# Optimization experiments

Hardware: AMD Instinct MI355X
Metric: run time of the kernel (lower is better)

Reference implementation:

```python
import jax, jax.numpy as jnp
import numpy as np

EMB_DIM = 2048
N_HEADS = 16
HEAD_DIM = EMB_DIM // N_HEADS
B, S = 4, 2048


def setup_inputs() -> dict:
    key = jax.random.key(0)
    kx, kq, kk, kv, ko = jax.random.split(key, 5)
    scale = 0.02
    return {
        "x": jax.random.normal(kx, (B, S, EMB_DIM), dtype=jnp.float32),
        "Wq": jax.random.normal(kq, (EMB_DIM, EMB_DIM), dtype=jnp.float32) * scale,
        "Wk": jax.random.normal(kk, (EMB_DIM, EMB_DIM), dtype=jnp.float32) * scale,
        "Wv": jax.random.normal(kv, (EMB_DIM, EMB_DIM), dtype=jnp.float32) * scale,
        "Wo": jax.random.normal(ko, (EMB_DIM, EMB_DIM), dtype=jnp.float32) * scale,
        "bo": jnp.zeros((EMB_DIM,), dtype=jnp.float32),
    }


def _split_heads(t):
    # [B, S, E] -> [B, H, S, Dh]
    b, s, _ = t.shape
    return t.reshape(b, s, N_HEADS, HEAD_DIM).transpose(0, 2, 1, 3)


def reference(x, Wq, Wk, Wv, Wo, bo):
    # torch nn.Linear: y = x @ W.T (no bias for qkv, bias for out_proj)
    q = _split_heads(x @ Wq.T)  # [B, H, S, Dh]
    k = _split_heads(x @ Wk.T)
    v = _split_heads(x @ Wv.T)

    scores = jnp.einsum("bhqd,bhkd->bhqk", q, k)  # [B, H, S, S]
    q_pos = jnp.arange(S)
    k_pos = jnp.arange(S)
    causal_mask = q_pos[:, None] < k_pos[None, :]  # True => future token, masked
    scores = jnp.where(causal_mask, -jnp.inf, scores)
    attn = jax.nn.softmax(scores / np.sqrt(HEAD_DIM).astype(np.float32), axis=-1)
    # dropout rate 0 (eval) -> identity
    ctx = jnp.einsum("bhqk,bhkd->bhqd", attn, v)  # [B, H, S, Dh]
    ctx = ctx.transpose(0, 2, 1, 3).reshape(B, S, EMB_DIM)
    return ctx @ Wo.T + bo
```

## Files before the change

### kernel.cpp

```cpp
#include <hip/hip_runtime.h>
#include <math.h>

#define EMB 2048
#define HD 128
#define SEQ 2048
#define MTOT 8192

typedef __bf16 bf16x8 __attribute__((ext_vector_type(8)));
typedef float floatx4 __attribute__((ext_vector_type(4)));

__device__ __forceinline__ unsigned short f2bf(float f) {
    unsigned u = __float_as_uint(f);
    return (unsigned short)((u + 0x7FFFu + ((u >> 16) & 1u)) >> 16);
}

__device__ __forceinline__ void gl_lds16(const void* g, void* lds) {
    __builtin_amdgcn_global_load_lds(
        (const __attribute__((address_space(1))) unsigned int*)g,
        (__attribute__((address_space(3))) unsigned int*)lds,
        16, 0, 0);
}

__global__ void cast_all_kernel(const float* __restrict__ x,
                                const float* __restrict__ w0,
                                const float* __restrict__ w1,
                                const float* __restrict__ w2,
                                const float* __restrict__ w3,
                                unsigned short* __restrict__ xb,
                                unsigned short* __restrict__ wb0,
                                unsigned short* __restrict__ wb1,
                                unsigned short* __restrict__ wb2,
                                unsigned short* __restrict__ wb3)
{
    const int XN4 = MTOT * EMB / 4;
    const int WN4 = EMB * EMB / 4;
    int i = blockIdx.x * blockDim.x + threadIdx.x;
    const float* src; unsigned short* dst; int off;
    if (i < XN4) { src = x; dst = xb; off = i; }
    else {
        int j = i - XN4;
        int wsel = j >> 20;
        off = j & (WN4 - 1);
        switch (wsel) {
            case 0: src = w0; dst = wb0; break;
            case 1: src = w1; dst = wb1; break;
            case 2: src = w2; dst = wb2; break;
            default: src = w3; dst = wb3; break;
        }
    }
    float4 v = reinterpret_cast<const float4*>(src)[off];
    ushort4 o;
    o.x = f2bf(v.x); o.y = f2bf(v.y); o.z = f2bf(v.z); o.w = f2bf(v.w);
    reinterpret_cast<ushort4*>(dst)[off] = o;
}

template<bool OUT_F32>
__global__ __launch_bounds__(256, 2)
void gemm_bt(const unsigned short* __restrict__ A,
             const unsigned short* __restrict__ Bw0,
             const unsigned short* __restrict__ Bw1,
             const unsigned short* __restrict__ Bw2,
             void* __restrict__ Cout0,
             void* __restrict__ Cout1,
             void* __restrict__ Cout2,
             const float* __restrict__ bias,
             int M, int N, int K, float scale0)
{
    __shared__ __align__(16) unsigned short sA[128][32];
    __shared__ __align__(16) unsigned short sB[128][32];

    const unsigned short* Bw = (blockIdx.z == 0) ? Bw0 : (blockIdx.z == 1) ? Bw1 : Bw2;
    void* Cout = (blockIdx.z == 0) ? Cout0 : (blockIdx.z == 1) ? Cout1 : Cout2;
    const float osc = (blockIdx.z == 0) ? scale0 : 1.0f;

    const int tid  = threadIdx.x;
    const int lane = tid & 63;
    const int wave = tid >> 6;
    const int wm = wave >> 1, wn = wave & 1;
    const int col  = lane & 15;
    const int quad = lane >> 4;

    const int m0 = blockIdx.y * 128;
    const int n0 = blockIdx.x * 128;

    floatx4 acc[4][4];
    #pragma unroll
    for (int i = 0; i < 4; i++)
        #pragma unroll
        for (int j = 0; j < 4; j++)
            #pragma unroll
            for (int r = 0; r < 4; r++) acc[i][j][r] = 0.0f;

    for (int k0 = 0; k0 < K; k0 += 32) {
        #pragma unroll
        for (int i = 0; i < 2; i++) {
            int c = tid + i * 256;
            int row = c >> 2, cc = (c & 3) * 8;
            char* ldsA = (char*)sA + (size_t)(i * 256 + wave * 64) * 16;
            char* ldsB = (char*)sB + (size_t)(i * 256 + wave * 64) * 16;
            gl_lds16(A  + (size_t)(m0 + row) * K + k0 + cc, ldsA);
            gl_lds16(Bw + (size_t)(n0 + row) * K + k0 + cc, ldsB);
        }
        __syncthreads();

        bf16x8 af[4], bfr[4];
        #pragma unroll
        for (int mi = 0; mi < 4; mi++)
            af[mi] = *reinterpret_cast<const bf16x8*>(&sA[wm*64 + mi*16 + col][quad*8]);
        #pragma unroll
        for (int ni = 0; ni < 4; ni++)
            bfr[ni] = *reinterpret_cast<const bf16x8*>(&sB[wn*64 + ni*16 + col][quad*8]);

        #pragma unroll
        for (int mi = 0; mi < 4; mi++)
            #pragma unroll
            for (int ni = 0; ni < 4; ni++)
                acc[mi][ni] = __builtin_amdgcn_mfma_f32_16x16x32_bf16(
                                  af[mi], bfr[ni], acc[mi][ni], 0, 0, 0);
        __syncthreads();
    }

    #pragma unroll
    for (int mi = 0; mi < 4; mi++) {
        #pragma unroll
        for (int ni = 0; ni < 4; ni++) {
            #pragma unroll
            for (int r = 0; r < 4; r++) {
                int row = m0 + wm*64 + mi*16 + quad*4 + r;
                int cg  = n0 + wn*64 + ni*16 + col;
                float v = acc[mi][ni][r];
                if (OUT_F32) {
                    float bb = bias ? bias[cg] : 0.0f;
                    reinterpret_cast<float*>(Cout)[(size_t)row * N + cg] = v + bb;
                } else {
                    reinterpret_cast<unsigned short*>(Cout)[(size_t)row * N + cg] = f2bf(v * osc);
                }
            }
        }
    }
}

__global__ __launch_bounds__(256, 2)
void flash_attn(const unsigned short* __restrict__ Q,
                const unsigned short* __restrict__ Kg,
                const unsigned short* __restrict__ Vg,
                unsigned short* __restrict__ O)
{
    __shared__ __align__(16) unsigned short sK[64 * 128];
    __shared__ __align__(16) unsigned short sVt[128][72];
    __shared__ __align__(16) unsigned short sP[4][16 * 72];

    const int tid  = threadIdx.x;
    const int lane = tid & 63;
    const int w    = tid >> 6;
    const int col  = lane & 15;
    const int quad = lane >> 4;

    const int h = blockIdx.y;
    const int b = blockIdx.z;
    const size_t rowbase = (size_t)b * SEQ;
    const int hoff = h * HD;

    unsigned short* sPw = sP[w];

    const int vk4 = (tid & 15) * 4;
    const int vd0 = (tid >> 4) * 8;

    #pragma unroll
    for (int phase = 0; phase < 2; phase++) {
        const int qsb = phase ? (int)blockIdx.x : (SEQ/128 - 1) - (int)blockIdx.x;
        const int qbase = qsb * 128;
        const int qg0 = qbase + w*32 + col;
        const int qg1 = qg0 + 16;

        bf16x8 qf[2][4];
        {
            const unsigned short* qr0 = Q + (rowbase + qg0) * EMB + hoff;
            const unsigned short* qr1 = Q + (rowbase + qg1) * EMB + hoff;
            #pragma unroll
            for (int ks = 0; ks < 4; ks++) {
                qf[0][ks] = *reinterpret_cast<const bf16x8*>(qr0 + ks*32 + quad*8);
                qf[1][ks] = *reinterpret_cast<const bf16x8*>(qr1 + ks*32 + quad*8);
            }
        }

        floatx4 oacc[2][8];
        #pragma unroll
        for (int g = 0; g < 2; g++)
            #pragma unroll
            for (int ni = 0; ni < 8; ni++)
                #pragma unroll
                for (int r = 0; r < 4; r++) oacc[g][ni][r] = 0.0f;
        float l_i[2] = {0.0f, 0.0f};

        const int ktmax = qbase / 64 + 1;
        for (int kt = 0; kt <= ktmax; kt++) {
            const int k0 = kt * 64;
            #pragma unroll
            for (int i = 0; i < 4; i++) {
                int c = tid + i * 256;
                int key = c >> 4;
                int dblk = (c & 15) ^ (key & 7);
                char* ldsK = (char*)sK + (size_t)(i * 256 + w * 64) * 16;
                gl_lds16(Kg + (rowbase + k0 + key) * EMB + hoff + dblk * 8, ldsK);
            }
            {
                unsigned short va[4][8];
                #pragma unroll
                for (int kk = 0; kk < 4; kk++)
                    *reinterpret_cast<int4*>(va[kk]) =
                        *reinterpret_cast<const int4*>(Vg + (rowbase + k0 + vk4 + kk) * EMB + hoff + vd0);
                #pragma unroll
                for (int j = 0; j < 8; j++) {
                    ushort4 o;
                    o.x = va[0][j]; o.y = va[1][j]; o.z = va[2][j]; o.w = va[3][j];
                    *reinterpret_cast<ushort4*>(&sVt[vd0 + j][vk4]) = o;
                }
            }
            __syncthreads();

            if (k0 <= qbase + w*32 + 31) {
                floatx4 sc[2][4];
                #pragma unroll
                for (int g = 0; g < 2; g++)
                    #pragma unroll
                    for (int ni = 0; ni < 4; ni++)
                        #pragma unroll
                        for (int r = 0; r < 4; r++) sc[g][ni][r] = 0.0f;
                #pragma unroll
                for (int ni = 0; ni < 4; ni++) {
                    #pragma unroll
                    for (int ks = 0; ks < 4; ks++) {
                        int u = (ni*16 + col) * 16 + ((ks*4 + quad) ^ (col & 7));
                        bf16x8 kf = *reinterpret_cast<const bf16x8*>(&sK[u * 8]);
                        sc[0][ni] = __builtin_amdgcn_mfma_f32_16x16x32_bf16(kf, qf[0][ks], sc[0][ni], 0, 0, 0);
                        sc[1][ni] = __builtin_amdgcn_mfma_f32_16x16x32_bf16(kf, qf[1][ks], sc[1][ni], 0, 0, 0);
                    }
                }

                const bool need_mask = (k0 + 63 > qbase + w*32);
                bf16x8 pf[2][2];

                #pragma unroll
                for (int g = 0; g < 2; g++) {
                    const int qg = (g == 0) ? qg0 : qg1;
                    if (need_mask) {
                        #pragma unroll
                        for (int ni = 0; ni < 4; ni++)
                            #pragma unroll
                            for (int r = 0; r < 4; r++) {
                                int key = k0 + ni*16 + quad*4 + r;
                                if (key > qg) sc[g][ni][r] = -1e30f;
                            }
                    }
                    float rsum = 0.0f;
                    #pragma unroll
                    for (int ni = 0; ni < 4; ni++) {
                        float p0 = __expf(sc[g][ni][0]);
                        float p1 = __expf(sc[g][ni][1]);
                        float p2 = __expf(sc[g][ni][2]);
                        float p3 = __expf(sc[g][ni][3]);
                        rsum += (p0 + p1) + (p2 + p3);
                        ushort4 pk;
                        pk.x = f2bf(p0); pk.y = f2bf(p1); pk.z = f2bf(p2); pk.w = f2bf(p3);
                        *reinterpret_cast<ushort4*>(&sPw[col*72 + ni*16 + quad*4]) = pk;
                    }
                    l_i[g] += rsum;
                    #pragma unroll
                    for (int ks = 0; ks < 2; ks++)
                        pf[g][ks] = *reinterpret_cast<const bf16x8*>(&sPw[col*72 + ks*32 + quad*8]);
                }

                #pragma unroll
                for (int ni = 0; ni < 8; ni++) {
                    #pragma unroll
                    for (int ks = 0; ks < 2; ks++) {
                        bf16x8 vf = *reinterpret_cast<const bf16x8*>(&sVt[ni*16 + col][ks*32 + quad*8]);
                        oacc[0][ni] = __builtin_amdgcn_mfma_f32_16x16x32_bf16(vf, pf[0][ks], oacc[0][ni], 0, 0, 0);
                        oacc[1][ni] = __builtin_amdgcn_mfma_f32_16x16x32_bf16(vf, pf[1][ks], oacc[1][ni], 0, 0, 0);
                    }
                }
            }
            __syncthreads();
        }

        #pragma unroll
        for (int g = 0; g < 2; g++) {
            const int qg = (g == 0) ? qg0 : qg1;
            float l = l_i[g];
            l += __shfl_xor(l, 16);
            l += __shfl_xor(l, 32);
            float inv = 1.0f / l;
            #pragma unroll
            for (int ni = 0; ni < 8; ni++) {
                ushort4 o4;
                o4.x = f2bf(oacc[g][ni][0] * inv);
                o4.y = f2bf(oacc[g][ni][1] * inv);
                o4.z = f2bf(oacc[g][ni][2] * inv);
                o4.w = f2bf(oacc[g][ni][3] * inv);
                *reinterpret_cast<ushort4*>(O + (rowbase + qg) * EMB + hoff + ni*16 + quad*4) = o4;
            }
        }
    }
}

extern "C" void kernel_launch(void* const* d_in, const int* in_sizes, int n_in,
                              void* d_out, int out_size, void* d_ws, size_t ws_size,
                              hipStream_t stream)
{
    const float* x  = (const float*)d_in[0];
    const float* Wq = (const float*)d_in[1];
    const float* Wk = (const float*)d_in[2];
    const float* Wv = (const float*)d_in[3];
    const float* Wo = (const float*)d_in[4];
    const float* bo = (const float*)d_in[5];
    float* out = (float*)d_out;

    unsigned short* ws = (unsigned short*)d_ws;
    const size_t XN = (size_t)MTOT * EMB;
    const size_t WN = (size_t)EMB * EMB;
    unsigned short* xb  = ws;
    unsigned short* wqb = xb  + XN;
    unsigned short* wkb = wqb + WN;
    unsigned short* wvb = wkb + WN;
    unsigned short* wob = wvb + WN;
    unsigned short* qb  = wob + WN;
    unsigned short* kb  = qb  + XN;
    unsigned short* vb  = kb  + XN;
    unsigned short* ctx = xb;

    {
        int total4 = (int)(XN/4 + 4*(WN/4));
        cast_all_kernel<<<total4 / 256, 256, 0, stream>>>(
            x, Wq, Wk, Wv, Wo, xb, wqb, wkb, wvb, wob);
    }

    const float scl = 0.08838834764831845f;
    gemm_bt<false><<<dim3(EMB/128, MTOT/128, 3), 256, 0, stream>>>(
        xb, wqb, wkb, wvb, qb, kb, vb, nullptr, MTOT, EMB, EMB, scl);

    flash_attn<<<dim3(SEQ/128/2, 16, 4), 256, 0, stream>>>(qb, kb, vb, ctx);

    gemm_bt<true><<<dim3(EMB/128, MTOT/128, 1), 256, 0, stream>>>(
        ctx, wob, nullptr, nullptr, out, nullptr, nullptr, bo, MTOT, EMB, EMB, 1.0f);
}
```

Before: 597.6 us.

## Rewrite projection GEMMs as 256x256 double-buffered pipelined kernels with swizzled LDS

```diff
diff --git a/kernel.cpp b/kernel.cpp
--- a/kernel.cpp
+++ b/kernel.cpp
@@ -54,20 +54,36 @@
     reinterpret_cast<ushort4*>(dst)[off] = o;
 }
 
+
+#define PH_PRE()  do { asm volatile("s_barrier" ::: "memory");               \
+                       asm volatile("s_waitcnt lgkmcnt(0)" ::: "memory");    \
+                       __builtin_amdgcn_sched_barrier(0);                    \
+                       __builtin_amdgcn_s_setprio(1); } while (0)
+#define PH_POST() do { __builtin_amdgcn_s_setprio(0);                        \
+                       asm volatile("s_barrier" ::: "memory"); } while (0)
+
+#define MFMA16(AF, BF, MI0)                                                  \
+    _Pragma("unroll")                                                        \
+    for (int mi = 0; mi < 4; mi++)                                           \
+        _Pragma("unroll")                                                    \
+        for (int ni = 0; ni < 4; ni++)                                       \
+            acc[(MI0) + mi][ni] = __builtin_amdgcn_mfma_f32_16x16x32_bf16(   \
+                AF[(MI0) + mi], BF[ni], acc[(MI0) + mi][ni], 0, 0, 0);
+
 template<bool OUT_F32>
-__global__ __launch_bounds__(256, 2)
-void gemm_bt(const unsigned short* __restrict__ A,
-             const unsigned short* __restrict__ Bw0,
-             const unsigned short* __restrict__ Bw1,
-             const unsigned short* __restrict__ Bw2,
-             void* __restrict__ Cout0,
-             void* __restrict__ Cout1,
-             void* __restrict__ Cout2,
-             const float* __restrict__ bias,
-             int M, int N, int K, float scale0)
+__global__ __launch_bounds__(512, 2)
+void gemm256_bt(const unsigned short* __restrict__ A,
+                const unsigned short* __restrict__ Bw0,
+                const unsigned short* __restrict__ Bw1,
+                const unsigned short* __restrict__ Bw2,
+                void* __restrict__ Cout0,
+                void* __restrict__ Cout1,
+                void* __restrict__ Cout2,
+                const float* __restrict__ bias,
+                int M, int N, int K, float scale0)
 {
-    __shared__ __align__(16) unsigned short sA[128][32];
-    __shared__ __align__(16) unsigned short sB[128][32];
+    __shared__ __align__(16) unsigned short sA[2][256][64];
+    __shared__ __align__(16) unsigned short sB[2][256][64];
 
     const unsigned short* Bw = (blockIdx.z == 0) ? Bw0 : (blockIdx.z == 1) ? Bw1 : Bw2;
     void* Cout = (blockIdx.z == 0) ? Cout0 : (blockIdx.z == 1) ? Cout1 : Cout2;
@@ -76,58 +92,145 @@
     const int tid  = threadIdx.x;
     const int lane = tid & 63;
     const int wave = tid >> 6;
-    const int wm = wave >> 1, wn = wave & 1;
+    const int wm   = wave >> 2;
+    const int wn   = wave & 3;
     const int col  = lane & 15;
     const int quad = lane >> 4;
 
-    const int m0 = blockIdx.y * 128;
-    const int n0 = blockIdx.x * 128;
-
-    floatx4 acc[4][4];
+    const int m0 = blockIdx.y * 256;
+    const int n0 = blockIdx.x * 256;
+
+    const int NT     = K >> 6;
+    const int NITER  = NT >> 1;
+    const int fourNT = NT << 2;
+
+    int sr[2], sc[2];
     #pragma unroll
-    for (int i = 0; i < 4; i++)
+    for (int q = 0; q < 2; q++) {
+        int P = (tid + (q << 9)) << 4;
+        int r = P >> 7;
+        sr[q] = r;
+        sc[q] = ((P & 127) ^ ((r & 7) << 4)) >> 1;
+    }
+
+    floatx4 acc[8][4];
+    #pragma unroll
+    for (int i = 0; i < 8; i++)
         #pragma unroll
         for (int j = 0; j < 4; j++)
             #pragma unroll
             for (int r = 0; r < 4; r++) acc[i][j][r] = 0.0f;
 
-    for (int k0 = 0; k0 < K; k0 += 32) {
-        #pragma unroll
-        for (int i = 0; i < 2; i++) {
-            int c = tid + i * 256;
-            int row = c >> 2, cc = (c & 3) * 8;
-            char* ldsA = (char*)sA + (size_t)(i * 256 + wave * 64) * 16;
-            char* ldsB = (char*)sB + (size_t)(i * 256 + wave * 64) * 16;
-            gl_lds16(A  + (size_t)(m0 + row) * K + k0 + cc, ldsA);
-            gl_lds16(Bw + (size_t)(n0 + row) * K + k0 + cc, ldsB);
-        }
-        __syncthreads();
-
-        bf16x8 af[4], bfr[4];
-        #pragma unroll
-        for (int mi = 0; mi < 4; mi++)
-            af[mi] = *reinterpret_cast<const bf16x8*>(&sA[wm*64 + mi*16 + col][quad*8]);
-        #pragma unroll
-        for (int ni = 0; ni < 4; ni++)
-            bfr[ni] = *reinterpret_cast<const bf16x8*>(&sB[wn*64 + ni*16 + col][quad*8]);
-
-        #pragma unroll
-        for (int mi = 0; mi < 4; mi++)
-            #pragma unroll
-            for (int ni = 0; ni < 4; ni++)
-                acc[mi][ni] = __builtin_amdgcn_mfma_f32_16x16x32_bf16(
-                                  af[mi], bfr[ni], acc[mi][ni], 0, 0, 0);
-        __syncthreads();
-    }
+    auto STAGE = [&](int s) {
+        if (s >= fourNT) return;
+        int t = s >> 2, j = s & 3;
+        int buf = t & 1;
+        int k0 = t << 6;
+        const unsigned short* src;
+        unsigned short* region;
+        int row0;
+        if (j < 2) { src = A;  region = &sA[buf][j << 7][0];       row0 = m0 + (j << 7); }
+        else       { src = Bw; region = &sB[buf][(j - 2) << 7][0]; row0 = n0 + ((j - 2) << 7); }
+        #pragma unroll
+        for (int q = 0; q < 2; q++) {
+            char* ldsb = (char*)region + (((wave << 6) + (q << 9)) << 4);
+            gl_lds16(src + (size_t)(row0 + sr[q]) * K + (k0 + sc[q]), ldsb);
+        }
+    };
+
+    const char* sAc = (const char*)&sA[0][0][0];
+    const char* sBc = (const char*)&sB[0][0][0];
+    auto LDA = [&](int buf, int mi, int kk) -> bf16x8 {
+        int R  = (wm << 7) + (mi << 4) + col;
+        int lo = (R << 7) + (kk << 6) + (quad << 4);
+        int po = lo ^ ((R & 7) << 4);
+        return *reinterpret_cast<const bf16x8*>(sAc + (buf << 15) + po);
+    };
+    auto LDB = [&](int buf, int ni, int kk) -> bf16x8 {
+        int R  = (wn << 6) + (ni << 4) + col;
+        int lo = (R << 7) + (kk << 6) + (quad << 4);
+        int po = lo ^ ((R & 7) << 4);
+        return *reinterpret_cast<const bf16x8*>(sBc + (buf << 15) + po);
+    };
 
     #pragma unroll
-    for (int mi = 0; mi < 4; mi++) {
+    for (int s = 0; s < 6; s++) STAGE(s);
+    asm volatile("s_waitcnt vmcnt(4)" ::: "memory");
+    asm volatile("s_barrier" ::: "memory");
+
+    #pragma unroll 1
+    for (int it = 0; it < NITER; ++it) {
+        const int sbase = 5 + (it << 3);
+        bf16x8 af0[8], af1[8], bf0[4], bf1[4];
+
+        #pragma unroll
+        for (int mi = 0; mi < 8; mi++) af0[mi] = LDA(0, mi, 0);
+        #pragma unroll
+        for (int ni = 0; ni < 4; ni++) bf0[ni] = LDB(0, ni, 0);
+        STAGE(sbase + 1);
+        PH_PRE();
+        MFMA16(af0, bf0, 0);
+        PH_POST();
+
+        #pragma unroll
+        for (int mi = 0; mi < 8; mi++) af1[mi] = LDA(0, mi, 1);
+        STAGE(sbase + 2);
+        PH_PRE();
+        MFMA16(af0, bf0, 4);
+        PH_POST();
+
+        #pragma unroll
+        for (int ni = 0; ni < 4; ni++) bf1[ni] = LDB(0, ni, 1);
+        STAGE(sbase + 3);
+        PH_PRE();
+        MFMA16(af1, bf1, 0);
+        PH_POST();
+
+        STAGE(sbase + 4);
+        if (it < NITER - 1) { asm volatile("s_waitcnt vmcnt(4)" ::: "memory"); }
+        else                { asm volatile("s_waitcnt vmcnt(0)" ::: "memory"); }
+        PH_PRE();
+        MFMA16(af1, bf1, 4);
+        PH_POST();
+
+        #pragma unroll
+        for (int mi = 0; mi < 8; mi++) af0[mi] = LDA(1, mi, 0);
+        #pragma unroll
+        for (int ni = 0; ni < 4; ni++) bf0[ni] = LDB(1, ni, 0);
+        STAGE(sbase + 5);
+        PH_PRE();
+        MFMA16(af0, bf0, 0);
+        PH_POST();
+
+        #pragma unroll
+        for (int mi = 0; mi < 8; mi++) af1[mi] = LDA(1, mi, 1);
+        STAGE(sbase + 6);
+        PH_PRE();
+        MFMA16(af0, bf0, 4);
+        PH_POST();
+
+        #pragma unroll
+        for (int ni = 0; ni < 4; ni++) bf1[ni] = LDB(1, ni, 1);
+        STAGE(sbase + 7);
+        PH_PRE();
+        MFMA16(af1, bf1, 0);
+        PH_POST();
+
+        STAGE(sbase + 8);
+        asm volatile("s_waitcnt vmcnt(4)" ::: "memory");
+        PH_PRE();
+        MFMA16(af1, bf1, 4);
+        PH_POST();
+    }
+
+    #pragma unroll
+    for (int mi = 0; mi < 8; mi++) {
         #pragma unroll
         for (int ni = 0; ni < 4; ni++) {
             #pragma unroll
             for (int r = 0; r < 4; r++) {
-                int row = m0 + wm*64 + mi*16 + quad*4 + r;
-                int cg  = n0 + wn*64 + ni*16 + col;
+                int row = m0 + (wm << 7) + (mi << 4) + (quad << 2) + r;
+                int cg  = n0 + (wn << 6) + (ni << 4) + col;
                 float v = acc[mi][ni][r];
                 if (OUT_F32) {
                     float bb = bias ? bias[cg] : 0.0f;
@@ -336,11 +439,11 @@
     }
 
     const float scl = 0.08838834764831845f;
-    gemm_bt<false><<<dim3(EMB/128, MTOT/128, 3), 256, 0, stream>>>(
+    gemm256_bt<false><<<dim3(EMB/256, MTOT/256, 3), 512, 0, stream>>>(
         xb, wqb, wkb, wvb, qb, kb, vb, nullptr, MTOT, EMB, EMB, scl);
 
     flash_attn<<<dim3(SEQ/128/2, 16, 4), 256, 0, stream>>>(qb, kb, vb, ctx);
 
-    gemm_bt<true><<<dim3(EMB/128, MTOT/128, 1), 256, 0, stream>>>(
+    gemm256_bt<true><<<dim3(EMB/256, MTOT/256, 1), 512, 0, stream>>>(
         ctx, wob, nullptr, nullptr, out, nullptr, nullptr, bo, MTOT, EMB, EMB, 1.0f);
 }
```

Result: slower. 1.275 ms (+113.3%).
